# Kernel tuning notes

Measured on AMD Instinct MI355X. Metric: run time of the kernel, lower is better.

Reference implementation:

```python
import jax, jax.numpy as jnp
import numpy as np

B, S, D, H = 2, 2048, 1024, 16
DK = D // H  # 64


def setup_inputs() -> dict:
    key = jax.random.key(0)
    ks = jax.random.split(key, 9)
    query = jax.random.normal(ks[0], (B, S, D), dtype=jnp.float32)
    k_in = jax.random.normal(ks[1], (B, S, D), dtype=jnp.float32)
    v_in = jax.random.normal(ks[2], (B, S, D), dtype=jnp.float32)
    mask = jax.random.randint(ks[3], (B, S, S), 0, 2, dtype=jnp.int32)
    sc = 1.0 / np.sqrt(D)
    Wq = jax.random.normal(ks[4], (H, D, DK), dtype=jnp.float32) * sc  # per-head q proj
    Wk = jax.random.normal(ks[5], (H, D, DK), dtype=jnp.float32) * sc
    Wv = jax.random.normal(ks[6], (H, D, DK), dtype=jnp.float32) * sc
    Wu = jax.random.normal(ks[7], (D, D), dtype=jnp.float32) * sc  # unifyheads weight
    bu = jax.random.normal(ks[8], (D,), dtype=jnp.float32) * 0.01
    return {"query": query, "key": k_in, "value": v_in, "mask": mask,
            "Wq": Wq, "Wk": Wk, "Wv": Wv, "Wu": Wu, "bu": bu}


def reference(query, key, value, mask, Wq, Wk, Wv, Wu, bu):
    scale = DK ** 0.25  # original divides q and k each by d_k^(1/4)
    q = jnp.einsum('bsd,hdk->bhsk', query, Wq) / scale
    k = jnp.einsum('bsd,hdk->bhsk', key, Wk) / scale
    v = jnp.einsum('bsd,hdk->bhsk', value, Wv)
    scores = jnp.einsum('bhsk,bhtk->bhst', q, k)  # [B,H,S,S]
    scores = jnp.where(mask[:, None, :, :] == 0, jnp.float32(-1e9), scores)
    attn = jax.nn.softmax(scores, axis=-1)
    out = jnp.einsum('bhst,bhtk->bhsk', attn, v)
    out = jnp.transpose(out, (0, 2, 1, 3)).reshape(query.shape[0], query.shape[1], D)  # concat heads
    return out @ Wu + bu
```

## Files before the change

### kernel.cpp

```cpp
#include <hip/hip_runtime.h>
#include <hip/hip_bf16.h>


typedef __bf16 bf16_t;
typedef __attribute__((ext_vector_type(4))) __bf16 bf16x4;
typedef __attribute__((ext_vector_type(8))) __bf16 bf16x8;
typedef __attribute__((ext_vector_type(4))) float f32x4;
typedef unsigned int u32;

#define B_ 2
#define S_ 2048
#define D_ 1024
#define H_ 16
#define DK_ 64
#define NX_ (4096 * 1024)

static __device__ __forceinline__ f32x4 mfma16(bf16x8 a, bf16x8 b, f32x4 c) {
  return __builtin_amdgcn_mfma_f32_16x16x32_bf16(a, b, c, 0, 0, 0);
}

static __device__ __forceinline__ void async16(const bf16_t* g, bf16_t* l) {
  __builtin_amdgcn_global_load_lds(
      (const __attribute__((address_space(1))) u32*)g,
      (__attribute__((address_space(3))) u32*)l, 16, 0, 0);
}

__global__ __launch_bounds__(256) void cvt_x(const float* __restrict__ q,
                                             const float* __restrict__ k,
                                             const float* __restrict__ v,
                                             bf16_t* __restrict__ qo,
                                             bf16_t* __restrict__ ko,
                                             bf16_t* __restrict__ vo) {
  const int z = blockIdx.y;
  const float* src = (z == 0) ? q : (z == 1) ? k : v;
  bf16_t* dst = (z == 0) ? qo : (z == 1) ? ko : vo;
  size_t i = ((size_t)blockIdx.x * 256 + threadIdx.x) * 8;
  float4 a = *(const float4*)(src + i);
  float4 b = *(const float4*)(src + i + 4);
  bf16x8 o;
  o[0] = (bf16_t)a.x; o[1] = (bf16_t)a.y; o[2] = (bf16_t)a.z; o[3] = (bf16_t)a.w;
  o[4] = (bf16_t)b.x; o[5] = (bf16_t)b.y; o[6] = (bf16_t)b.z; o[7] = (bf16_t)b.w;
  *(bf16x8*)(dst + i) = o;
}

__global__ __launch_bounds__(256) void wtrans(
    const float* __restrict__ Wq, const float* __restrict__ Wk,
    const float* __restrict__ Wv, const float* __restrict__ Wu,
    bf16_t* __restrict__ Bq, bf16_t* __restrict__ Bk,
    bf16_t* __restrict__ Bv, bf16_t* __restrict__ Bu, float qkscale) {
  __shared__ __align__(16) bf16_t T[64][72];
  const int z = blockIdx.z;
  const float* W = (z == 0) ? Wq : (z == 1) ? Wk : (z == 2) ? Wv : Wu;
  bf16_t* BT = (z == 0) ? Bq : (z == 1) ? Bk : (z == 2) ? Bv : Bu;
  const float scale = (z <= 1) ? qkscale : 1.0f;
  const int d0 = blockIdx.x * 64, nt = blockIdx.y;
  const int tid = threadIdx.x;
  const int r = tid & 63, g = tid >> 6;

  const float* src = (z < 3)
      ? W + ((size_t)nt * D_ + d0 + r) * DK_ + g * 16
      : W + (size_t)(d0 + r) * D_ + nt * 64 + g * 16;
#pragma unroll
  for (int j = 0; j < 4; ++j) {
    float4 w4 = *(const float4*)(src + j * 4);
    T[g * 16 + j * 4 + 0][r] = (bf16_t)(w4.x * scale);
    T[g * 16 + j * 4 + 1][r] = (bf16_t)(w4.y * scale);
    T[g * 16 + j * 4 + 2][r] = (bf16_t)(w4.z * scale);
    T[g * 16 + j * 4 + 3][r] = (bf16_t)(w4.w * scale);
  }
  __syncthreads();
  const int orow = tid >> 3, seg = tid & 7;
#pragma unroll
  for (int p = 0; p < 2; ++p) {
    int rr = p * 32 + orow;
    *(bf16x8*)(BT + (size_t)(nt * 64 + rr) * D_ + d0 + seg * 8) =
        *(const bf16x8*)&T[rr][seg * 8];
  }
}

__global__ __launch_bounds__(256) void vt_build(const bf16_t* __restrict__ V,
                                                bf16_t* __restrict__ Vt) {
  __shared__ __align__(16) bf16_t T[64][72];
  const int r0 = blockIdx.x * 64;
  const int c0 = blockIdx.y * 64;
  const int tid = threadIdx.x;
#pragma unroll
  for (int it = 0; it < 2; ++it) {
    int t = tid + it * 256;
    int rr = t >> 3, cc = (t & 7) * 8;
    *(bf16x8*)&T[rr][cc] = *(const bf16x8*)(V + (size_t)(r0 + rr) * D_ + c0 + cc);
  }
  __syncthreads();
#pragma unroll
  for (int it = 0; it < 2; ++it) {
    int t = tid + it * 256;
    int cr = t >> 3, rc = (t & 7) * 8;
    bf16x8 v;
#pragma unroll
    for (int j = 0; j < 8; ++j) v[j] = T[rc + j][cr];
    *(bf16x8*)(Vt + (size_t)(c0 + cr) * 4096 + r0 + rc) = v;
  }
}

__global__ __launch_bounds__(256) void mask_pack(const int* __restrict__ mask,
                                                 unsigned int* __restrict__ bits) {
  int w = blockIdx.x * 256 + threadIdx.x;
  const int4* p = (const int4*)(mask + (size_t)w * 32);
  unsigned int v = 0;
#pragma unroll
  for (int i = 0; i < 8; ++i) {
    int4 m4 = p[i];
    v |= (m4.x != 0 ? 1u : 0u) << (i * 4 + 0);
    v |= (m4.y != 0 ? 1u : 0u) << (i * 4 + 1);
    v |= (m4.z != 0 ? 1u : 0u) << (i * 4 + 2);
    v |= (m4.w != 0 ? 1u : 0u) << (i * 4 + 3);
  }
  bits[w] = v;
}

__global__ __launch_bounds__(256) void gemm_bt(
    const bf16_t* __restrict__ A0, const bf16_t* __restrict__ A1,
    const bf16_t* __restrict__ A2, const bf16_t* __restrict__ BT0,
    const bf16_t* __restrict__ BT1, const bf16_t* __restrict__ BT2,
    bf16_t* __restrict__ C0, bf16_t* __restrict__ C1, bf16_t* __restrict__ C2) {
  __shared__ __align__(16) bf16_t As[128 * 64];
  __shared__ __align__(16) bf16_t Bs[128 * 64];

  const int z = blockIdx.z;
  const bf16_t* A = (z == 0) ? A0 : (z == 1) ? A1 : A2;
  const bf16_t* BT = (z == 0) ? BT0 : (z == 1) ? BT1 : BT2;
  bf16_t* C = (z == 0) ? C0 : (z == 1) ? C1 : C2;

  const int tid = threadIdx.x;
  const int lane = tid & 63, wave = tid >> 6;
  const int l = lane & 15, quad = lane >> 4;
  const int wm = wave >> 1, wn = wave & 1;
  const int row0 = blockIdx.x * 128, col0 = blockIdx.y * 128;

  const int lr = lane >> 3;
  const int gc8 = (lane & 7) ^ lr;
  const int xl = l & 7;

  f32x4 acc[4][4];
#pragma unroll
  for (int i = 0; i < 4; ++i)
#pragma unroll
    for (int j = 0; j < 4; ++j) acc[i][j] = {0.f, 0.f, 0.f, 0.f};

  for (int k0 = 0; k0 < 1024; k0 += 64) {
    __syncthreads();
#pragma unroll
    for (int c = 0; c < 4; ++c) {
      int r = wave * 32 + c * 8;
      async16(A + (size_t)(row0 + r + lr) * 1024 + k0 + gc8 * 8, As + r * 64);
      async16(BT + (size_t)(col0 + r + lr) * 1024 + k0 + gc8 * 8, Bs + r * 64);
    }
    __syncthreads();

#pragma unroll
    for (int kh = 0; kh < 2; ++kh) {
      bf16x8 af[4], bf[4];
#pragma unroll
      for (int f = 0; f < 4; ++f)
        af[f] = *(const bf16x8*)&As[(wm * 64 + f * 16 + l) * 64 +
                                    (((kh * 4 + quad) ^ xl) * 8)];
#pragma unroll
      for (int f = 0; f < 4; ++f)
        bf[f] = *(const bf16x8*)&Bs[(wn * 64 + f * 16 + l) * 64 +
                                    (((kh * 4 + quad) ^ xl) * 8)];
#pragma unroll
      for (int fm = 0; fm < 4; ++fm)
#pragma unroll
        for (int fn = 0; fn < 4; ++fn)
          acc[fm][fn] = mfma16(af[fm], bf[fn], acc[fm][fn]);
    }
  }

#pragma unroll
  for (int fm = 0; fm < 4; ++fm)
#pragma unroll
    for (int fn = 0; fn < 4; ++fn)
#pragma unroll
      for (int reg = 0; reg < 4; ++reg) {
        int row = row0 + wm * 64 + fm * 16 + quad * 4 + reg;
        int col = col0 + wn * 64 + fn * 16 + l;
        C[(size_t)row * 1024 + col] = (bf16_t)acc[fm][fn][reg];
      }
}

__global__ __launch_bounds__(256) void gemm_bt64(
    const bf16_t* __restrict__ A, const bf16_t* __restrict__ BT,
    float* __restrict__ C, const float* __restrict__ bias) {
  __shared__ __align__(16) bf16_t As[64 * 64];
  __shared__ __align__(16) bf16_t Bs[128 * 64];

  const int tid = threadIdx.x;
  const int lane = tid & 63, wave = tid >> 6;
  const int l = lane & 15, quad = lane >> 4;
  const int row0 = blockIdx.x * 64, col0 = blockIdx.y * 128;

  const int lr = lane >> 3;
  const int gc8 = (lane & 7) ^ lr;
  const int xl = l & 7;

  f32x4 acc[4][2];
#pragma unroll
  for (int i = 0; i < 4; ++i)
#pragma unroll
    for (int j = 0; j < 2; ++j) acc[i][j] = {0.f, 0.f, 0.f, 0.f};

  for (int k0 = 0; k0 < 1024; k0 += 64) {
    __syncthreads();
#pragma unroll
    for (int c = 0; c < 2; ++c) {
      int r = wave * 16 + c * 8;
      async16(A + (size_t)(row0 + r + lr) * 1024 + k0 + gc8 * 8, As + r * 64);
    }
#pragma unroll
    for (int c = 0; c < 4; ++c) {
      int r = wave * 32 + c * 8;
      async16(BT + (size_t)(col0 + r + lr) * 1024 + k0 + gc8 * 8, Bs + r * 64);
    }
    __syncthreads();

#pragma unroll
    for (int kh = 0; kh < 2; ++kh) {
      bf16x8 af[4], bf[2];
#pragma unroll
      for (int f = 0; f < 4; ++f)
        af[f] = *(const bf16x8*)&As[(f * 16 + l) * 64 +
                                    (((kh * 4 + quad) ^ xl) * 8)];
#pragma unroll
      for (int f = 0; f < 2; ++f)
        bf[f] = *(const bf16x8*)&Bs[(wave * 32 + f * 16 + l) * 64 +
                                    (((kh * 4 + quad) ^ xl) * 8)];
#pragma unroll
      for (int fm = 0; fm < 4; ++fm)
#pragma unroll
        for (int fn = 0; fn < 2; ++fn)
          acc[fm][fn] = mfma16(af[fm], bf[fn], acc[fm][fn]);
    }
  }

#pragma unroll
  for (int fm = 0; fm < 4; ++fm)
#pragma unroll
    for (int fn = 0; fn < 2; ++fn)
#pragma unroll
      for (int reg = 0; reg < 4; ++reg) {
        int row = row0 + fm * 16 + quad * 4 + reg;
        int col = col0 + wave * 32 + fn * 16 + l;
        C[(size_t)row * 1024 + col] = acc[fm][fn][reg] + bias[col];
      }
}

__global__ __launch_bounds__(128) void attn_kernel(
    const bf16_t* __restrict__ Qx, const bf16_t* __restrict__ Kx,
    const bf16_t* __restrict__ Vt, const unsigned int* __restrict__ mbits,
    bf16_t* __restrict__ out) {
  __shared__ __align__(16) bf16_t Ks[64 * 64];
  __shared__ __align__(16) bf16_t Vts[64 * 64];
  __shared__ __align__(16) bf16_t Ps[2][32][72];

  const int tid = threadIdx.x;
  const int lane = tid & 63, wave = tid >> 6;
  const int l = lane & 15, quad = lane >> 4;
  const int qt = blockIdx.x, h = blockIdx.y, b = blockIdx.z;
  const int ch = h * 64;
  const size_t rb = (size_t)b * S_;
  const int q0 = qt * 64 + wave * 32;

  const int lr = lane >> 3;
  const int gc8 = (lane & 7) ^ lr;
  const int xl = l & 7;

  bf16x8 bq[2][2];
#pragma unroll
  for (int mf = 0; mf < 2; ++mf) {
    const bf16_t* qp = Qx + (rb + q0 + mf * 16 + l) * D_ + ch;
    bq[mf][0] = *(const bf16x8*)(qp + quad * 8);
    bq[mf][1] = *(const bf16x8*)(qp + 32 + quad * 8);
  }

  const f32x4 zero = {0.f, 0.f, 0.f, 0.f};
  f32x4 o[2][4];
  float lsum[2] = {0.f, 0.f};
#pragma unroll
  for (int mf = 0; mf < 2; ++mf)
#pragma unroll
    for (int nt = 0; nt < 4; ++nt) o[mf][nt] = zero;

  const u32* mrow[2];
#pragma unroll
  for (int mf = 0; mf < 2; ++mf)
    mrow[mf] = mbits + (size_t)(b * S_ + q0 + mf * 16 + l) * (S_ / 32);

  for (int t0 = 0; t0 < S_; t0 += 64) {
    __syncthreads();
#pragma unroll
    for (int it = 0; it < 4; ++it) {
      int r0 = it * 16 + wave * 8;
      async16(Kx + (rb + t0 + r0 + lr) * D_ + ch + gc8 * 8, Ks + r0 * 64);
      async16(Vt + (size_t)(ch + r0 + lr) * 4096 + rb + t0 + gc8 * 8,
              Vts + r0 * 64);
    }
    __syncthreads();

#pragma unroll
    for (int mf = 0; mf < 2; ++mf) {
      u32 mw0 = mrow[mf][(t0 >> 5)];
      u32 mw1 = mrow[mf][(t0 >> 5) + 1];
#pragma unroll
      for (int ts = 0; ts < 4; ++ts) {
        int rK = (ts * 16 + l) * 64;
        bf16x8 ak0 = *(const bf16x8*)&Ks[rK + ((quad ^ xl) * 8)];
        bf16x8 ak1 = *(const bf16x8*)&Ks[rK + (((4 + quad) ^ xl) * 8)];
        f32x4 s = mfma16(ak0, bq[mf][0], zero);
        s = mfma16(ak1, bq[mf][1], s);

        u32 mw = (ts < 2) ? mw0 : mw1;
        u32 nib = (mw >> ((ts & 1) * 16 + quad * 4)) & 0xFu;
        bf16x4 pv;
#pragma unroll
        for (int reg = 0; reg < 4; ++reg) {
          float e = __expf(fminf(s[reg], 30.0f));
          float p = ((nib >> reg) & 1u) ? e : 0.0f;
          lsum[mf] += p;
          pv[reg] = (bf16_t)p;
        }
        *(bf16x4*)&Ps[wave][mf * 16 + l][ts * 16 + quad * 4] = pv;
      }
    }

    bf16x8 ap[2][2];
#pragma unroll
    for (int mf = 0; mf < 2; ++mf) {
      ap[mf][0] = *(const bf16x8*)&Ps[wave][mf * 16 + l][quad * 8];
      ap[mf][1] = *(const bf16x8*)&Ps[wave][mf * 16 + l][32 + quad * 8];
    }
#pragma unroll
    for (int nt = 0; nt < 4; ++nt) {
      int rV = (nt * 16 + l) * 64;
      bf16x8 bv0 = *(const bf16x8*)&Vts[rV + ((quad ^ xl) * 8)];
      bf16x8 bv1 = *(const bf16x8*)&Vts[rV + (((4 + quad) ^ xl) * 8)];
#pragma unroll
      for (int mf = 0; mf < 2; ++mf) {
        o[mf][nt] = mfma16(ap[mf][0], bv0, o[mf][nt]);
        o[mf][nt] = mfma16(ap[mf][1], bv1, o[mf][nt]);
      }
    }
  }

#pragma unroll
  for (int mf = 0; mf < 2; ++mf) {
    float rsum = lsum[mf];
    rsum += __shfl_xor(rsum, 16);
    rsum += __shfl_xor(rsum, 32);
    float inv = (rsum > 0.f) ? (1.f / rsum) : 0.f;
    float invr[4];
#pragma unroll
    for (int reg = 0; reg < 4; ++reg) invr[reg] = __shfl(inv, quad * 4 + reg);
#pragma unroll
    for (int reg = 0; reg < 4; ++reg) {
      int srow = q0 + mf * 16 + quad * 4 + reg;
      bf16_t* op = out + (rb + srow) * D_ + ch;
#pragma unroll
      for (int nt = 0; nt < 4; ++nt)
        op[nt * 16 + l] = (bf16_t)(o[mf][nt][reg] * invr[reg]);
    }
  }
}

extern "C" void kernel_launch(void* const* d_in, const int* in_sizes, int n_in,
                              void* d_out, int out_size, void* d_ws, size_t ws_size,
                              hipStream_t stream) {
  const float* q_in = (const float*)d_in[0];
  const float* k_in = (const float*)d_in[1];
  const float* v_in = (const float*)d_in[2];
  const int* mask = (const int*)d_in[3];
  const float* Wq = (const float*)d_in[4];
  const float* Wk = (const float*)d_in[5];
  const float* Wv = (const float*)d_in[6];
  const float* Wu = (const float*)d_in[7];
  const float* bu = (const float*)d_in[8];
  float* outp = (float*)d_out;

  bf16_t* qx = (bf16_t*)d_ws;
  bf16_t* kx = qx + NX_;
  bf16_t* vx = kx + NX_;
  bf16_t* qb = vx + NX_;
  bf16_t* kb = qb + NX_;
  bf16_t* vb = kb + NX_;
  bf16_t* BTq = vb + NX_;
  bf16_t* BTk = BTq + D_ * D_;
  bf16_t* BTv = BTk + D_ * D_;
  bf16_t* BTu = BTv + D_ * D_;
  unsigned int* mb = (unsigned int*)(BTu + D_ * D_);
  bf16_t* ab = qx;
  bf16_t* vtb = kx;

  const float qkscale = 0.35355339059327373f;

  dim3 blk(256);
  cvt_x<<<dim3(2048, 3), blk, 0, stream>>>(q_in, k_in, v_in, qx, kx, vx);
  wtrans<<<dim3(16, 16, 4), blk, 0, stream>>>(Wq, Wk, Wv, Wu, BTq, BTk, BTv, BTu, qkscale);
  mask_pack<<<dim3(1024), blk, 0, stream>>>(mask, mb);
  gemm_bt<<<dim3(32, 8, 3), blk, 0, stream>>>(qx, kx, vx, BTq, BTk, BTv,
                                              qb, kb, vb);
  vt_build<<<dim3(64, 16), blk, 0, stream>>>(vb, vtb);
  attn_kernel<<<dim3(S_ / 64, H_, B_), dim3(128), 0, stream>>>(qb, kb, vtb, mb, ab);
  gemm_bt64<<<dim3(64, 8), blk, 0, stream>>>(ab, BTu, outp, bu);
}
```

Before: 285.9 us.

## Use four waves per attention block, MFMA row sums, and exp2 with folded scale

The attention kernel now runs 256 threads per block, with each wave owning 16 query rows instead of 32. This halves per-wave register state and increases the number of waves per block. The softmax denominator now comes from an MFMA against a ones vector instead of scalar accumulation plus shuffles. exp2f replaces __expf, with log2(e) folded into the q/k projection scale, and masking uses a bitwise select. s_setprio raises priority around the PV MFMAs. The costs are that each K/V tile is reused by fewer query rows per wave, and the row sum is now taken from bf16-rounded probabilities.

Measured after the change: 285.6 us. No clear change (-0.1%).

```diff
diff --git a/kernel.cpp b/kernel.cpp
--- a/kernel.cpp
+++ b/kernel.cpp
@@ -254,13 +254,13 @@
       }
 }
 
-__global__ __launch_bounds__(128) void attn_kernel(
+__global__ __launch_bounds__(256, 4) void attn_kernel(
     const bf16_t* __restrict__ Qx, const bf16_t* __restrict__ Kx,
     const bf16_t* __restrict__ Vt, const unsigned int* __restrict__ mbits,
     bf16_t* __restrict__ out) {
   __shared__ __align__(16) bf16_t Ks[64 * 64];
   __shared__ __align__(16) bf16_t Vts[64 * 64];
-  __shared__ __align__(16) bf16_t Ps[2][32][72];
+  __shared__ __align__(16) bf16_t Ps[4][16][72];
 
   const int tid = threadIdx.x;
   const int lane = tid & 63, wave = tid >> 6;
@@ -268,106 +268,91 @@
   const int qt = blockIdx.x, h = blockIdx.y, b = blockIdx.z;
   const int ch = h * 64;
   const size_t rb = (size_t)b * S_;
-  const int q0 = qt * 64 + wave * 32;
+  const int q0 = qt * 64 + wave * 16;
 
   const int lr = lane >> 3;
   const int gc8 = (lane & 7) ^ lr;
   const int xl = l & 7;
 
-  bf16x8 bq[2][2];
-#pragma unroll
-  for (int mf = 0; mf < 2; ++mf) {
-    const bf16_t* qp = Qx + (rb + q0 + mf * 16 + l) * D_ + ch;
-    bq[mf][0] = *(const bf16x8*)(qp + quad * 8);
-    bq[mf][1] = *(const bf16x8*)(qp + 32 + quad * 8);
-  }
+  bf16x8 bq[2];
+  {
+    const bf16_t* qp = Qx + (rb + q0 + l) * D_ + ch;
+    bq[0] = *(const bf16x8*)(qp + quad * 8);
+    bq[1] = *(const bf16x8*)(qp + 32 + quad * 8);
+  }
+
+  bf16x8 ones;
+#pragma unroll
+  for (int j = 0; j < 8; ++j) ones[j] = (bf16_t)1.0f;
 
   const f32x4 zero = {0.f, 0.f, 0.f, 0.f};
-  f32x4 o[2][4];
-  float lsum[2] = {0.f, 0.f};
-#pragma unroll
-  for (int mf = 0; mf < 2; ++mf)
-#pragma unroll
-    for (int nt = 0; nt < 4; ++nt) o[mf][nt] = zero;
-
-  const u32* mrow[2];
-#pragma unroll
-  for (int mf = 0; mf < 2; ++mf)
-    mrow[mf] = mbits + (size_t)(b * S_ + q0 + mf * 16 + l) * (S_ / 32);
+  f32x4 o[4];
+  f32x4 rs = zero;
+#pragma unroll
+  for (int nt = 0; nt < 4; ++nt) o[nt] = zero;
+
+  const u32* mrow = mbits + (size_t)(b * S_ + q0 + l) * (S_ / 32);
 
   for (int t0 = 0; t0 < S_; t0 += 64) {
     __syncthreads();
 #pragma unroll
-    for (int it = 0; it < 4; ++it) {
-      int r0 = it * 16 + wave * 8;
+    for (int it = 0; it < 2; ++it) {
+      int r0 = it * 32 + wave * 8;
       async16(Kx + (rb + t0 + r0 + lr) * D_ + ch + gc8 * 8, Ks + r0 * 64);
       async16(Vt + (size_t)(ch + r0 + lr) * 4096 + rb + t0 + gc8 * 8,
               Vts + r0 * 64);
     }
     __syncthreads();
 
-#pragma unroll
-    for (int mf = 0; mf < 2; ++mf) {
-      u32 mw0 = mrow[mf][(t0 >> 5)];
-      u32 mw1 = mrow[mf][(t0 >> 5) + 1];
-#pragma unroll
-      for (int ts = 0; ts < 4; ++ts) {
-        int rK = (ts * 16 + l) * 64;
-        bf16x8 ak0 = *(const bf16x8*)&Ks[rK + ((quad ^ xl) * 8)];
-        bf16x8 ak1 = *(const bf16x8*)&Ks[rK + (((4 + quad) ^ xl) * 8)];
-        f32x4 s = mfma16(ak0, bq[mf][0], zero);
-        s = mfma16(ak1, bq[mf][1], s);
-
-        u32 mw = (ts < 2) ? mw0 : mw1;
-        u32 nib = (mw >> ((ts & 1) * 16 + quad * 4)) & 0xFu;
-        bf16x4 pv;
-#pragma unroll
-        for (int reg = 0; reg < 4; ++reg) {
-          float e = __expf(fminf(s[reg], 30.0f));
-          float p = ((nib >> reg) & 1u) ? e : 0.0f;
-          lsum[mf] += p;
-          pv[reg] = (bf16_t)p;
-        }
-        *(bf16x4*)&Ps[wave][mf * 16 + l][ts * 16 + quad * 4] = pv;
+    u32 mw0 = mrow[(t0 >> 5)];
+    u32 mw1 = mrow[(t0 >> 5) + 1];
+
+#pragma unroll
+    for (int ts = 0; ts < 4; ++ts) {
+      int rK = (ts * 16 + l) * 64;
+      bf16x8 ak0 = *(const bf16x8*)&Ks[rK + ((quad ^ xl) * 8)];
+      bf16x8 ak1 = *(const bf16x8*)&Ks[rK + (((4 + quad) ^ xl) * 8)];
+      f32x4 s = mfma16(ak0, bq[0], zero);
+      s = mfma16(ak1, bq[1], s);
+
+      u32 mw = (ts < 2) ? mw0 : mw1;
+      u32 nib = (mw >> ((ts & 1) * 16 + quad * 4)) & 0xFu;
+      bf16x4 pv;
+#pragma unroll
+      for (int reg = 0; reg < 4; ++reg) {
+        float e = exp2f(fminf(s[reg], 43.28f));
+        int bm = ((int)(nib << (31 - reg))) >> 31;
+        float p = __int_as_float(__float_as_int(e) & bm);
+        pv[reg] = (bf16_t)p;
       }
-    }
-
-    bf16x8 ap[2][2];
-#pragma unroll
-    for (int mf = 0; mf < 2; ++mf) {
-      ap[mf][0] = *(const bf16x8*)&Ps[wave][mf * 16 + l][quad * 8];
-      ap[mf][1] = *(const bf16x8*)&Ps[wave][mf * 16 + l][32 + quad * 8];
-    }
+      *(bf16x4*)&Ps[wave][l][ts * 16 + quad * 4] = pv;
+    }
+
+    bf16x8 ap0 = *(const bf16x8*)&Ps[wave][l][quad * 8];
+    bf16x8 ap1 = *(const bf16x8*)&Ps[wave][l][32 + quad * 8];
+
+    __builtin_amdgcn_s_setprio(1);
+    rs = mfma16(ap0, ones, rs);
+    rs = mfma16(ap1, ones, rs);
 #pragma unroll
     for (int nt = 0; nt < 4; ++nt) {
       int rV = (nt * 16 + l) * 64;
       bf16x8 bv0 = *(const bf16x8*)&Vts[rV + ((quad ^ xl) * 8)];
       bf16x8 bv1 = *(const bf16x8*)&Vts[rV + (((4 + quad) ^ xl) * 8)];
-#pragma unroll
-      for (int mf = 0; mf < 2; ++mf) {
-        o[mf][nt] = mfma16(ap[mf][0], bv0, o[mf][nt]);
-        o[mf][nt] = mfma16(ap[mf][1], bv1, o[mf][nt]);
-      }
-    }
-  }
-
-#pragma unroll
-  for (int mf = 0; mf < 2; ++mf) {
-    float rsum = lsum[mf];
-    rsum += __shfl_xor(rsum, 16);
-    rsum += __shfl_xor(rsum, 32);
-    float inv = (rsum > 0.f) ? (1.f / rsum) : 0.f;
-    float invr[4];
-#pragma unroll
-    for (int reg = 0; reg < 4; ++reg) invr[reg] = __shfl(inv, quad * 4 + reg);
-#pragma unroll
-    for (int reg = 0; reg < 4; ++reg) {
-      int srow = q0 + mf * 16 + quad * 4 + reg;
-      bf16_t* op = out + (rb + srow) * D_ + ch;
-#pragma unroll
-      for (int nt = 0; nt < 4; ++nt)
-        op[nt * 16 + l] = (bf16_t)(o[mf][nt][reg] * invr[reg]);
-    }
+      o[nt] = mfma16(ap0, bv0, o[nt]);
+      o[nt] = mfma16(ap1, bv1, o[nt]);
+    }
+    __builtin_amdgcn_s_setprio(0);
+  }
+
+#pragma unroll
+  for (int reg = 0; reg < 4; ++reg) {
+    float inv = (rs[reg] > 0.f) ? (1.f / rs[reg]) : 0.f;
+    int srow = q0 + quad * 4 + reg;
+    bf16_t* op = out + (rb + srow) * D_ + ch;
+#pragma unroll
+    for (int nt = 0; nt < 4; ++nt)
+      op[nt * 16 + l] = (bf16_t)(o[nt][reg] * inv);
   }
 }
 
@@ -399,7 +384,7 @@
   bf16_t* ab = qx;
   bf16_t* vtb = kx;
 
-  const float qkscale = 0.35355339059327373f;
+  const float qkscale = 0.35355339059327373f * 1.2011224087864498f;
 
   dim3 blk(256);
   cvt_x<<<dim3(2048, 3), blk, 0, stream>>>(q_in, k_in, v_in, qx, kx, vx);
@@ -408,6 +393,6 @@
   gemm_bt<<<dim3(32, 8, 3), blk, 0, stream>>>(qx, kx, vx, BTq, BTk, BTv,
                                               qb, kb, vb);
   vt_build<<<dim3(64, 16), blk, 0, stream>>>(vb, vtb);
-  attn_kernel<<<dim3(S_ / 64, H_, B_), dim3(128), 0, stream>>>(qb, kb, vtb, mb, ab);
+  attn_kernel<<<dim3(S_ / 64, H_, B_), dim3(256), 0, stream>>>(qb, kb, vtb, mb, ab);
   gemm_bt64<<<dim3(64, 8), blk, 0, stream>>>(ab, BTu, outp, bu);
 }
```
